# Optimization experiments

Measured on AMD Instinct MI355X. Metric: run time of the kernel, lower is better.

The kernel has to match this reference:

```python
import jax, jax.numpy as jnp
import numpy as np

N_NODES = 50000
N_EDGES = 800000
IN_DIM = 128
ADD = 8
HIDDEN = 256
OUT_DIM = 128


def gcn_conv(x, src, dst, W, b, n_nodes):
    """PyG GCNConv: linear -> sym-normalized scatter-add with self-loops -> bias."""
    loop = jnp.arange(n_nodes, dtype=src.dtype)
    s = jnp.concatenate([src, loop])
    d = jnp.concatenate([dst, loop])
    deg = jax.ops.segment_sum(jnp.ones(s.shape[0], dtype=x.dtype), d, num_segments=n_nodes)
    dinv = jnp.where(deg > 0, jax.lax.rsqrt(deg), 0.0)
    norm = dinv[s] * dinv[d]                       # [E+N]
    h = x @ W                                      # [N, F_out]
    msg = h[s] * norm[:, None]                     # [E+N, F_out]
    out = jax.ops.segment_sum(msg, d, num_segments=n_nodes)
    return out + b


def prelu(x, a):
    return jnp.where(x >= 0, x, a * x)


def setup_inputs() -> dict:
    key = jax.random.key(0)
    ks = jax.random.split(key, 8)
    x = jax.random.normal(ks[0], (N_NODES, IN_DIM), dtype=jnp.float32)
    edge_index = jax.random.randint(ks[1], (2, N_EDGES), 0, N_NODES, dtype=jnp.int64)
    id_vec = jax.random.normal(ks[2], (ADD,), dtype=jnp.float32)
    # Glorot-ish init for linear weights, PReLU slope 0.25 (torch default)
    W1 = jax.random.normal(ks[3], (IN_DIM + ADD, HIDDEN), dtype=jnp.float32) * 0.05
    b1 = jnp.zeros((HIDDEN,), dtype=jnp.float32)
    a1 = jnp.full((HIDDEN,), 0.25, dtype=jnp.float32)
    W2 = jax.random.normal(ks[4], (HIDDEN, OUT_DIM), dtype=jnp.float32) * 0.05
    b2 = jnp.zeros((OUT_DIM,), dtype=jnp.float32)
    a2 = jnp.full((OUT_DIM,), 0.25, dtype=jnp.float32)
    return {"x": x, "edge_index": edge_index, "id": id_vec,
            "W1": W1, "b1": b1, "a1": a1, "W2": W2, "b2": b2, "a2": a2}


def reference(x, edge_index, id, W1, b1, a1, W2, b2, a2):
    n = x.shape[0]
    src, dst = edge_index[0], edge_index[1]
    # tile id vector onto every node and concat along features
    xi = jnp.concatenate([x, jnp.broadcast_to(id[None, :], (n, id.shape[0]))], axis=1)
    h = gcn_conv(xi, src, dst, W1, b1, n)
    h = prelu(h, a1)
    h = gcn_conv(h, src, dst, W2, b2, n)
    h = prelu(h, a2)
    return h
```

## Files before the change

### kernel.cpp

```cpp
#include <hip/hip_runtime.h>


constexpr int NN = 50000;
constexpr int NE = 800000;
constexpr int NBUCK = 196;
constexpr int TILE = 2048;
constexpr int NSCAT = (NE + TILE - 1) / TILE;

typedef __attribute__((ext_vector_type(8))) short short8;
typedef __attribute__((ext_vector_type(4))) float floatx4;

__device__ inline void bsplit(float v, unsigned short& hi, unsigned short& lo) {
  unsigned u = __float_as_uint(v);
  hi = (unsigned short)(u >> 16);
  float rem = v - __uint_as_float(u & 0xffff0000u);
  lo = (unsigned short)(__float_as_uint(rem) >> 16);
}

__device__ inline unsigned short bf16_rtne(float v) {
  unsigned u = __float_as_uint(v);
  return (unsigned short)((u + 0x7fffu + ((u >> 16) & 1u)) >> 16);
}

__device__ inline float bflo(unsigned u) { return __uint_as_float(u << 16); }
__device__ inline float bfhi(unsigned u) { return __uint_as_float(u & 0xffff0000u); }


__global__ __launch_bounds__(256) void tile_count_kernel(const int* __restrict__ ei,
                                                         int* __restrict__ tilecnt) {
  __shared__ int h[NBUCK];
  int t = threadIdx.x;
  for (int i = t; i < NBUCK; i += 256) h[i] = 0;
  __syncthreads();
  int base = blockIdx.x * TILE;
  int end = base + TILE; if (end > NE) end = NE;
  for (int e = base + t; e < end; e += 256) atomicAdd(&h[ei[NE + e] >> 8], 1);
  __syncthreads();
  for (int i = t; i < NBUCK; i += 256) tilecnt[blockIdx.x * NBUCK + i] = h[i];
}

__global__ __launch_bounds__(256) void tile_scan_a_kernel(const int* __restrict__ tilecnt,
                                                          int* __restrict__ tpre,
                                                          int* __restrict__ bcnt) {
  __shared__ int sm[256];
  int b = blockIdx.x, t = threadIdx.x;
  int i0 = 2 * t, i1 = 2 * t + 1;
  int v0 = (i0 < NSCAT) ? tilecnt[i0 * NBUCK + b] : 0;
  int v1 = (i1 < NSCAT) ? tilecnt[i1 * NBUCK + b] : 0;
  int s = v0 + v1;
  sm[t] = s;
  __syncthreads();
  for (int off = 1; off < 256; off <<= 1) {
    int u = (t >= off) ? sm[t - off] : 0;
    __syncthreads();
    sm[t] += u;
    __syncthreads();
  }
  int ex = sm[t] - s;
  if (i0 < NSCAT) tpre[i0 * NBUCK + b] = ex;
  if (i1 < NSCAT) tpre[i1 * NBUCK + b] = ex + v0;
  if (t == 255) bcnt[b] = sm[255];
}

__global__ void bucket_base_kernel(const int* __restrict__ bcnt, int* __restrict__ bbase) {
  __shared__ int sm[256];
  int t = threadIdx.x;
  int v = (t < NBUCK) ? bcnt[t] : 0;
  sm[t] = v;
  __syncthreads();
  for (int off = 1; off < 256; off <<= 1) {
    int u = (t >= off) ? sm[t - off] : 0;
    __syncthreads();
    sm[t] += u;
    __syncthreads();
  }
  if (t < NBUCK) bbase[t] = sm[t] - v;
}

__global__ __launch_bounds__(256) void bucket_scatter_kernel(
    const int* __restrict__ ei, const int* __restrict__ tilecnt,
    const int* __restrict__ tpre, const int* __restrict__ bbase,
    unsigned* __restrict__ ebuf) {
  __shared__ int lbase[NBUCK], gb[NBUCK], lcur[NBUCK], ssc[256];
  __shared__ unsigned stage[TILE];
  int t = threadIdx.x;
  int tile = blockIdx.x;
  int base = tile * TILE;
  int cntTile = NE - base; if (cntTile > TILE) cntTile = TILE;
  int h = (t < NBUCK) ? tilecnt[tile * NBUCK + t] : 0;
  ssc[t] = h;
  __syncthreads();
  for (int off = 1; off < 256; off <<= 1) {
    int u = (t >= off) ? ssc[t - off] : 0;
    __syncthreads();
    ssc[t] += u;
    __syncthreads();
  }
  if (t < NBUCK) {
    int ex = ssc[t] - h;
    lbase[t] = ex;
    lcur[t] = ex;
    gb[t] = bbase[t] + tpre[tile * NBUCK + t];
  }
  __syncthreads();
  for (int e = base + t; e < base + cntTile; e += 256) {
    int s = ei[e];
    int d = ei[NE + e];
    int b = d >> 8;
    int pos = atomicAdd(&lcur[b], 1);
    stage[pos] = ((unsigned)(d & 255) << 16) | (unsigned)s;
  }
  __syncthreads();
  for (int i = t; i < cntTile; i += 256) {
    int lo = 0, hi = NBUCK - 1;
    while (lo < hi) {
      int mid = (lo + hi + 1) >> 1;
      if (lbase[mid] <= i) lo = mid; else hi = mid - 1;
    }
    ebuf[gb[lo] + (i - lbase[lo])] = stage[i];
  }
}

__global__ __launch_bounds__(256) void bucket_csr_kernel(
    const unsigned* __restrict__ ebuf, const int* __restrict__ bbase,
    const int* __restrict__ bcnt, int* __restrict__ offs, int* __restrict__ col,
    float* __restrict__ dinv) {
  __shared__ int cnt[256], cur[256], sums[256];
  int b = blockIdx.x, t = threadIdx.x;
  int node0 = b << 8;
  cnt[t] = 0;
  __syncthreads();
  int g0 = bbase[b], g1 = g0 + bcnt[b];
  for (int i = g0 + t; i < g1; i += 256) atomicAdd(&cnt[ebuf[i] >> 16], 1);
  __syncthreads();
  int c = cnt[t];
  sums[t] = c;
  __syncthreads();
  for (int off = 1; off < 256; off <<= 1) {
    int u = (t >= off) ? sums[t - off] : 0;
    __syncthreads();
    sums[t] += u;
    __syncthreads();
  }
  int ex = sums[t] - c;
  cur[t] = ex;
  int node = node0 + t;
  if (node < NN) {
    offs[node] = g0 + ex;
    dinv[node] = rsqrtf((float)(c + 1));
  }
  __syncthreads();
  for (int i = g0 + t; i < g1; i += 256) {
    unsigned v = ebuf[i];
    int pos = atomicAdd(&cur[v >> 16], 1);
    col[g0 + pos] = (int)(v & 0xffffu);
  }
  if (b == 0 && t == 0) offs[NN] = NE;
}

__global__ __launch_bounds__(256) void post_csr_kernel(
    const float* __restrict__ x, const float* __restrict__ dinv,
    const int* __restrict__ offs, const int* __restrict__ col,
    unsigned short* __restrict__ xsb, float* __restrict__ Svec) {
  int id = blockIdx.x * 256 + threadIdx.x;
  if (id < NN * 32) {
    float dd = dinv[id >> 5];
    float4 v = ((const float4*)x)[id];
    ushort4 o;
    o.x = bf16_rtne(v.x * dd);
    o.y = bf16_rtne(v.y * dd);
    o.z = bf16_rtne(v.z * dd);
    o.w = bf16_rtne(v.w * dd);
    ((ushort4*)xsb)[id] = o;
  } else {
    int d = id - NN * 32;
    if (d < NN) {
      float s = 0.f;
      int end = offs[d + 1];
      for (int p = offs[d]; p < end; ++p) s += dinv[col[p]];
      float dd = dinv[d];
      Svec[d] = dd * (dd + s);
    }
  }
}

template <int K, int N>
__device__ inline void pack_one(const float* __restrict__ W, unsigned short* __restrict__ Bhi,
                                unsigned short* __restrict__ Blo, int id) {
  constexpr int KC = K / 32;
  int j = id & 7;
  int lane = (id >> 3) & 63;
  int rest = id >> 9;
  int c = rest % KC;
  int nt = rest / KC;
  int k = c * 32 + (lane >> 4) * 8 + j;
  int n = nt * 16 + (lane & 15);
  unsigned short hi, lo;
  bsplit(W[(size_t)k * N + n], hi, lo);
  Bhi[id] = hi;
  Blo[id] = lo;
}

__global__ void prep_weights_kernel(const float* __restrict__ W1, const float* __restrict__ W2,
                                    const float* __restrict__ idv,
                                    unsigned short* __restrict__ B1hi, unsigned short* __restrict__ B1lo,
                                    unsigned short* __restrict__ B2hi, unsigned short* __restrict__ B2lo,
                                    float* __restrict__ cvec) {
  int id = blockIdx.x * 256 + threadIdx.x;
  if (id < 32768) {
    pack_one<128, 256>(W1, B1hi, B1lo, id);
  } else if (id < 65536) {
    pack_one<256, 128>(W2, B2hi, B2lo, id - 32768);
  } else if (id < 65536 + 256) {
    int m = id - 65536;
    float c = 0.f;
#pragma unroll
    for (int j = 0; j < 8; ++j) c += idv[j] * W1[(128 + j) * 256 + m];
    cvec[m] = c;
  }
}

template <int MODE>
__global__ __launch_bounds__(256) void agg_kernel(
    const unsigned short* __restrict__ in, const float* __restrict__ dinv,
    const int* __restrict__ offs, const int* __restrict__ col,
    const float* __restrict__ bias, const float* __restrict__ alpha,
    unsigned short* __restrict__ outhi, unsigned short* __restrict__ outlo,
    float* __restrict__ outf) {
  const uint2* inb = (const uint2*)in;
  int t = threadIdx.x;
  int node = blockIdx.x * 4 + (t >> 6);
  int lane = t & 63;
  int r = lane & 31;
  int half = lane >> 5;
  int beg = offs[node], end = offs[node + 1];

  float4 a0 = make_float4(0.f, 0.f, 0.f, 0.f);
  float4 a1 = make_float4(0.f, 0.f, 0.f, 0.f);
  float4 a2 = make_float4(0.f, 0.f, 0.f, 0.f);
  float4 a3 = make_float4(0.f, 0.f, 0.f, 0.f);
  int p = beg + half;
  for (; p + 14 < end; p += 16) {
    int s0 = col[p];      int s1 = col[p + 2];
    int s2 = col[p + 4];  int s3 = col[p + 6];
    int s4 = col[p + 8];  int s5 = col[p + 10];
    int s6 = col[p + 12]; int s7 = col[p + 14];
    uint2 v0 = inb[(size_t)s0 * 32 + r];
    uint2 v1 = inb[(size_t)s1 * 32 + r];
    uint2 v2 = inb[(size_t)s2 * 32 + r];
    uint2 v3 = inb[(size_t)s3 * 32 + r];
    uint2 v4 = inb[(size_t)s4 * 32 + r];
    uint2 v5 = inb[(size_t)s5 * 32 + r];
    uint2 v6 = inb[(size_t)s6 * 32 + r];
    uint2 v7 = inb[(size_t)s7 * 32 + r];
    a0.x += bflo(v0.x); a0.y += bfhi(v0.x); a0.z += bflo(v0.y); a0.w += bfhi(v0.y);
    a1.x += bflo(v1.x); a1.y += bfhi(v1.x); a1.z += bflo(v1.y); a1.w += bfhi(v1.y);
    a2.x += bflo(v2.x); a2.y += bfhi(v2.x); a2.z += bflo(v2.y); a2.w += bfhi(v2.y);
    a3.x += bflo(v3.x); a3.y += bfhi(v3.x); a3.z += bflo(v3.y); a3.w += bfhi(v3.y);
    a0.x += bflo(v4.x); a0.y += bfhi(v4.x); a0.z += bflo(v4.y); a0.w += bfhi(v4.y);
    a1.x += bflo(v5.x); a1.y += bfhi(v5.x); a1.z += bflo(v5.y); a1.w += bfhi(v5.y);
    a2.x += bflo(v6.x); a2.y += bfhi(v6.x); a2.z += bflo(v6.y); a2.w += bfhi(v6.y);
    a3.x += bflo(v7.x); a3.y += bfhi(v7.x); a3.z += bflo(v7.y); a3.w += bfhi(v7.y);
  }
  for (; p + 2 < end; p += 4) {
    int s0 = col[p];
    int s1 = col[p + 2];
    uint2 v0 = inb[(size_t)s0 * 32 + r];
    uint2 v1 = inb[(size_t)s1 * 32 + r];
    a0.x += bflo(v0.x); a0.y += bfhi(v0.x); a0.z += bflo(v0.y); a0.w += bfhi(v0.y);
    a1.x += bflo(v1.x); a1.y += bfhi(v1.x); a1.z += bflo(v1.y); a1.w += bfhi(v1.y);
  }
  if (p < end) {
    uint2 v0 = inb[(size_t)col[p] * 32 + r];
    a0.x += bflo(v0.x); a0.y += bfhi(v0.x); a0.z += bflo(v0.y); a0.w += bfhi(v0.y);
  }
  float4 acc = make_float4((a0.x + a1.x) + (a2.x + a3.x), (a0.y + a1.y) + (a2.y + a3.y),
                           (a0.z + a1.z) + (a2.z + a3.z), (a0.w + a1.w) + (a2.w + a3.w));
  acc.x += __shfl_xor(acc.x, 32);
  acc.y += __shfl_xor(acc.y, 32);
  acc.z += __shfl_xor(acc.z, 32);
  acc.w += __shfl_xor(acc.w, 32);

  float dd = dinv[node];
  if (half == 0) {
    uint2 sv = inb[(size_t)node * 32 + r];
    acc.x = dd * (acc.x + bflo(sv.x));
    acc.y = dd * (acc.y + bfhi(sv.x));
    acc.z = dd * (acc.z + bflo(sv.y));
    acc.w = dd * (acc.w + bfhi(sv.y));
    if (MODE == 0) {
      ushort4 h4, l4;
      bsplit(acc.x, h4.x, l4.x);
      bsplit(acc.y, h4.y, l4.y);
      bsplit(acc.z, h4.z, l4.z);
      bsplit(acc.w, h4.w, l4.w);
      ((ushort4*)outhi)[(size_t)node * 32 + r] = h4;
      ((ushort4*)outlo)[(size_t)node * 32 + r] = l4;
    } else {
      float4 b = ((const float4*)bias)[r];
      float4 al = ((const float4*)alpha)[r];
      acc.x += b.x; acc.y += b.y; acc.z += b.z; acc.w += b.w;
      acc.x = (acc.x >= 0.f) ? acc.x : al.x * acc.x;
      acc.y = (acc.y >= 0.f) ? acc.y : al.y * acc.y;
      acc.z = (acc.z >= 0.f) ? acc.z : al.z * acc.z;
      acc.w = (acc.w >= 0.f) ? acc.w : al.w * acc.w;
      ((float4*)outf)[(size_t)node * 32 + r] = acc;
    }
  }
}

__global__ __launch_bounds__(256) void gemm_fused_kernel(
    const unsigned short* __restrict__ Ahi, const unsigned short* __restrict__ Alo,
    const unsigned short* __restrict__ B1hi, const unsigned short* __restrict__ B1lo,
    const unsigned short* __restrict__ B2hi, const unsigned short* __restrict__ B2lo,
    const float* __restrict__ Svec, const float* __restrict__ cvec,
    const float* __restrict__ bias, const float* __restrict__ alpha,
    const float* __restrict__ dinv, unsigned short* __restrict__ h2b) {
  constexpr int K1 = 128, KC1 = 4, NT1 = 16;
  constexpr int KC2 = 8, NT2 = 8;
  __shared__ __attribute__((aligned(16))) char smem[4 * 16384];

  int wave = threadIdx.x >> 6;
  int lane = threadIdx.x & 63;
  int row0 = blockIdx.x * 64 + wave * 16;
  if (row0 >= NN) return;
  int m = lane & 15, quad = lane >> 4;
  char* wb = smem + wave * 16384;

  short8 ah[KC1], al[KC1];
  const unsigned short* ap = Ahi + (size_t)(row0 + m) * K1 + quad * 8;
  const unsigned short* alp = Alo + (size_t)(row0 + m) * K1 + quad * 8;
#pragma unroll
  for (int c = 0; c < KC1; ++c) {
    ah[c] = *(const short8*)(ap + c * 32);
    al[c] = *(const short8*)(alp + c * 32);
  }
  float sv[4];
#pragma unroll
  for (int i = 0; i < 4; ++i) sv[i] = Svec[row0 + quad * 4 + i];

#pragma unroll 1
  for (int nt = 0; nt < NT1; ++nt) {
    floatx4 acc = {0.f, 0.f, 0.f, 0.f};
#pragma unroll
    for (int c = 0; c < KC1; ++c) {
      short8 bh = *(const short8*)(B1hi + ((size_t)(nt * KC1 + c) * 64 + lane) * 8);
      short8 bl = *(const short8*)(B1lo + ((size_t)(nt * KC1 + c) * 64 + lane) * 8);
      acc = __builtin_amdgcn_mfma_f32_16x16x32_bf16(ah[c], bh, acc, 0, 0, 0);
      acc = __builtin_amdgcn_mfma_f32_16x16x32_bf16(ah[c], bl, acc, 0, 0, 0);
      acc = __builtin_amdgcn_mfma_f32_16x16x32_bf16(al[c], bh, acc, 0, 0, 0);
    }
    int c0 = nt * 16 + m;
    float cv = cvec[c0], bb = bias[c0], aa = alpha[c0];
#pragma unroll
    for (int i = 0; i < 4; ++i) {
      float v = acc[i] + sv[i] * cv + bb;
      v = (v >= 0.f) ? v : aa * v;
      unsigned short hi, lo;
      bsplit(v, hi, lo);
      int row16 = quad * 4 + i;
      int off = row16 * 512 + ((c0 * 2) ^ ((row16 & 7) << 4));
      *(unsigned short*)(wb + off) = hi;
      *(unsigned short*)(wb + 8192 + off) = lo;
    }
  }

  short8 ah2[KC2], al2[KC2];
#pragma unroll
  for (int c = 0; c < KC2; ++c) {
    int off = m * 512 + ((c * 64 + quad * 16) ^ ((m & 7) << 4));
    ah2[c] = *(const short8*)(wb + off);
    al2[c] = *(const short8*)(wb + 8192 + off);
  }
  float dv[4];
#pragma unroll
  for (int i = 0; i < 4; ++i) dv[i] = dinv[row0 + quad * 4 + i];

#pragma unroll 1
  for (int nt = 0; nt < NT2; ++nt) {
    floatx4 acc = {0.f, 0.f, 0.f, 0.f};
#pragma unroll
    for (int c = 0; c < KC2; ++c) {
      short8 bh = *(const short8*)(B2hi + ((size_t)(nt * KC2 + c) * 64 + lane) * 8);
      short8 bl = *(const short8*)(B2lo + ((size_t)(nt * KC2 + c) * 64 + lane) * 8);
      acc = __builtin_amdgcn_mfma_f32_16x16x32_bf16(ah2[c], bh, acc, 0, 0, 0);
      acc = __builtin_amdgcn_mfma_f32_16x16x32_bf16(ah2[c], bl, acc, 0, 0, 0);
      acc = __builtin_amdgcn_mfma_f32_16x16x32_bf16(al2[c], bh, acc, 0, 0, 0);
    }
    int c0 = nt * 16 + m;
#pragma unroll
    for (int i = 0; i < 4; ++i) {
      int r = row0 + quad * 4 + i;
      h2b[(size_t)r * 128 + c0] = bf16_rtne(acc[i] * dv[i]);
    }
  }
}

extern "C" void kernel_launch(void* const* d_in, const int* in_sizes, int n_in,
                              void* d_out, int out_size, void* d_ws, size_t ws_size,
                              hipStream_t stream) {
  const float* x = (const float*)d_in[0];
  const int* ei = (const int*)d_in[1];
  const float* idv = (const float*)d_in[2];
  const float* W1 = (const float*)d_in[3];
  const float* b1 = (const float*)d_in[4];
  const float* a1 = (const float*)d_in[5];
  const float* W2 = (const float*)d_in[6];
  const float* b2 = (const float*)d_in[7];
  const float* a2 = (const float*)d_in[8];
  float* out = (float*)d_out;

  char* w = (char*)d_ws;
  size_t off = 0;
  auto alloc = [&](size_t bytes) -> void* {
    void* p = w + off;
    off += bytes;
    off = (off + 255) & ~(size_t)255;
    return p;
  };
  int* tilecnt = (int*)alloc((size_t)NSCAT * NBUCK * 4);
  int* tpre = (int*)alloc((size_t)NSCAT * NBUCK * 4);
  int* bbase = (int*)alloc((size_t)NBUCK * 4);
  int* bcnt = (int*)alloc((size_t)NBUCK * 4);
  unsigned* ebuf = (unsigned*)alloc((size_t)NE * 4);
  float* dinv = (float*)alloc((size_t)NN * 4);
  float* Svec = (float*)alloc((size_t)NN * 4);
  int* offs = (int*)alloc((size_t)(NN + 1) * 4);
  int* col = (int*)alloc((size_t)NE * 4);
  float* cvec = (float*)alloc(256 * 4);
  unsigned short* xsb = (unsigned short*)alloc((size_t)NN * 128 * 2);
  unsigned short* aggxhi = (unsigned short*)alloc((size_t)NN * 128 * 2);
  unsigned short* aggxlo = (unsigned short*)alloc((size_t)NN * 128 * 2);
  unsigned short* h2b = (unsigned short*)alloc((size_t)NN * 128 * 2);
  unsigned short* B1hi = (unsigned short*)alloc(128 * 256 * 2);
  unsigned short* B1lo = (unsigned short*)alloc(128 * 256 * 2);
  unsigned short* B2hi = (unsigned short*)alloc(256 * 128 * 2);
  unsigned short* B2lo = (unsigned short*)alloc(256 * 128 * 2);

  tile_count_kernel<<<NSCAT, 256, 0, stream>>>(ei, tilecnt);
  tile_scan_a_kernel<<<NBUCK, 256, 0, stream>>>(tilecnt, tpre, bcnt);
  bucket_base_kernel<<<1, 256, 0, stream>>>(bcnt, bbase);
  bucket_scatter_kernel<<<NSCAT, 256, 0, stream>>>(ei, tilecnt, tpre, bbase, ebuf);
  bucket_csr_kernel<<<NBUCK, 256, 0, stream>>>(ebuf, bbase, bcnt, offs, col, dinv);

  prep_weights_kernel<<<(65536 + 256 + 255) / 256, 256, 0, stream>>>(
      W1, W2, idv, B1hi, B1lo, B2hi, B2lo, cvec);
  post_csr_kernel<<<(NN * 32 + NN + 255) / 256, 256, 0, stream>>>(
      x, dinv, offs, col, xsb, Svec);

  agg_kernel<0><<<NN / 4, 256, 0, stream>>>(xsb, dinv, offs, col, nullptr, nullptr,
                                            aggxhi, aggxlo, nullptr);

  gemm_fused_kernel<<<(NN + 63) / 64, 256, 0, stream>>>(
      aggxhi, aggxlo, B1hi, B1lo, B2hi, B2lo, Svec, cvec, b1, a1, dinv, h2b);

  agg_kernel<1><<<NN / 4, 256, 0, stream>>>(h2b, dinv, offs, col, b2, a2,
                                            nullptr, nullptr, out);
}
```

Measured before the change: 256.4 us.

## Fuse graph preprocessing kernels to cut launches and intermediate passes

Folds weight packing into the tile-count kernel and replaces the separate bucket-base scan with a redundant in-block scan of bucket counts inside the scatter and CSR kernels. The x-scaling and bf16 conversion moves into the bucket CSR kernel, which reads dinv from shared memory, and the Svec computation moves into the first aggregation kernel. This removes three kernel launches and their serialization gaps. In exchange, the x conversion now runs on only 196 blocks with a non-unrolled loop, which may lower memory-level parallelism for that pass.

```diff
diff --git a/kernel.cpp b/kernel.cpp
--- a/kernel.cpp
+++ b/kernel.cpp
@@ -24,165 +24,6 @@
 
 __device__ inline float bflo(unsigned u) { return __uint_as_float(u << 16); }
 __device__ inline float bfhi(unsigned u) { return __uint_as_float(u & 0xffff0000u); }
-
-
-__global__ __launch_bounds__(256) void tile_count_kernel(const int* __restrict__ ei,
-                                                         int* __restrict__ tilecnt) {
-  __shared__ int h[NBUCK];
-  int t = threadIdx.x;
-  for (int i = t; i < NBUCK; i += 256) h[i] = 0;
-  __syncthreads();
-  int base = blockIdx.x * TILE;
-  int end = base + TILE; if (end > NE) end = NE;
-  for (int e = base + t; e < end; e += 256) atomicAdd(&h[ei[NE + e] >> 8], 1);
-  __syncthreads();
-  for (int i = t; i < NBUCK; i += 256) tilecnt[blockIdx.x * NBUCK + i] = h[i];
-}
-
-__global__ __launch_bounds__(256) void tile_scan_a_kernel(const int* __restrict__ tilecnt,
-                                                          int* __restrict__ tpre,
-                                                          int* __restrict__ bcnt) {
-  __shared__ int sm[256];
-  int b = blockIdx.x, t = threadIdx.x;
-  int i0 = 2 * t, i1 = 2 * t + 1;
-  int v0 = (i0 < NSCAT) ? tilecnt[i0 * NBUCK + b] : 0;
-  int v1 = (i1 < NSCAT) ? tilecnt[i1 * NBUCK + b] : 0;
-  int s = v0 + v1;
-  sm[t] = s;
-  __syncthreads();
-  for (int off = 1; off < 256; off <<= 1) {
-    int u = (t >= off) ? sm[t - off] : 0;
-    __syncthreads();
-    sm[t] += u;
-    __syncthreads();
-  }
-  int ex = sm[t] - s;
-  if (i0 < NSCAT) tpre[i0 * NBUCK + b] = ex;
-  if (i1 < NSCAT) tpre[i1 * NBUCK + b] = ex + v0;
-  if (t == 255) bcnt[b] = sm[255];
-}
-
-__global__ void bucket_base_kernel(const int* __restrict__ bcnt, int* __restrict__ bbase) {
-  __shared__ int sm[256];
-  int t = threadIdx.x;
-  int v = (t < NBUCK) ? bcnt[t] : 0;
-  sm[t] = v;
-  __syncthreads();
-  for (int off = 1; off < 256; off <<= 1) {
-    int u = (t >= off) ? sm[t - off] : 0;
-    __syncthreads();
-    sm[t] += u;
-    __syncthreads();
-  }
-  if (t < NBUCK) bbase[t] = sm[t] - v;
-}
-
-__global__ __launch_bounds__(256) void bucket_scatter_kernel(
-    const int* __restrict__ ei, const int* __restrict__ tilecnt,
-    const int* __restrict__ tpre, const int* __restrict__ bbase,
-    unsigned* __restrict__ ebuf) {
-  __shared__ int lbase[NBUCK], gb[NBUCK], lcur[NBUCK], ssc[256];
-  __shared__ unsigned stage[TILE];
-  int t = threadIdx.x;
-  int tile = blockIdx.x;
-  int base = tile * TILE;
-  int cntTile = NE - base; if (cntTile > TILE) cntTile = TILE;
-  int h = (t < NBUCK) ? tilecnt[tile * NBUCK + t] : 0;
-  ssc[t] = h;
-  __syncthreads();
-  for (int off = 1; off < 256; off <<= 1) {
-    int u = (t >= off) ? ssc[t - off] : 0;
-    __syncthreads();
-    ssc[t] += u;
-    __syncthreads();
-  }
-  if (t < NBUCK) {
-    int ex = ssc[t] - h;
-    lbase[t] = ex;
-    lcur[t] = ex;
-    gb[t] = bbase[t] + tpre[tile * NBUCK + t];
-  }
-  __syncthreads();
-  for (int e = base + t; e < base + cntTile; e += 256) {
-    int s = ei[e];
-    int d = ei[NE + e];
-    int b = d >> 8;
-    int pos = atomicAdd(&lcur[b], 1);
-    stage[pos] = ((unsigned)(d & 255) << 16) | (unsigned)s;
-  }
-  __syncthreads();
-  for (int i = t; i < cntTile; i += 256) {
-    int lo = 0, hi = NBUCK - 1;
-    while (lo < hi) {
-      int mid = (lo + hi + 1) >> 1;
-      if (lbase[mid] <= i) lo = mid; else hi = mid - 1;
-    }
-    ebuf[gb[lo] + (i - lbase[lo])] = stage[i];
-  }
-}
-
-__global__ __launch_bounds__(256) void bucket_csr_kernel(
-    const unsigned* __restrict__ ebuf, const int* __restrict__ bbase,
-    const int* __restrict__ bcnt, int* __restrict__ offs, int* __restrict__ col,
-    float* __restrict__ dinv) {
-  __shared__ int cnt[256], cur[256], sums[256];
-  int b = blockIdx.x, t = threadIdx.x;
-  int node0 = b << 8;
-  cnt[t] = 0;
-  __syncthreads();
-  int g0 = bbase[b], g1 = g0 + bcnt[b];
-  for (int i = g0 + t; i < g1; i += 256) atomicAdd(&cnt[ebuf[i] >> 16], 1);
-  __syncthreads();
-  int c = cnt[t];
-  sums[t] = c;
-  __syncthreads();
-  for (int off = 1; off < 256; off <<= 1) {
-    int u = (t >= off) ? sums[t - off] : 0;
-    __syncthreads();
-    sums[t] += u;
-    __syncthreads();
-  }
-  int ex = sums[t] - c;
-  cur[t] = ex;
-  int node = node0 + t;
-  if (node < NN) {
-    offs[node] = g0 + ex;
-    dinv[node] = rsqrtf((float)(c + 1));
-  }
-  __syncthreads();
-  for (int i = g0 + t; i < g1; i += 256) {
-    unsigned v = ebuf[i];
-    int pos = atomicAdd(&cur[v >> 16], 1);
-    col[g0 + pos] = (int)(v & 0xffffu);
-  }
-  if (b == 0 && t == 0) offs[NN] = NE;
-}
-
-__global__ __launch_bounds__(256) void post_csr_kernel(
-    const float* __restrict__ x, const float* __restrict__ dinv,
-    const int* __restrict__ offs, const int* __restrict__ col,
-    unsigned short* __restrict__ xsb, float* __restrict__ Svec) {
-  int id = blockIdx.x * 256 + threadIdx.x;
-  if (id < NN * 32) {
-    float dd = dinv[id >> 5];
-    float4 v = ((const float4*)x)[id];
-    ushort4 o;
-    o.x = bf16_rtne(v.x * dd);
-    o.y = bf16_rtne(v.y * dd);
-    o.z = bf16_rtne(v.z * dd);
-    o.w = bf16_rtne(v.w * dd);
-    ((ushort4*)xsb)[id] = o;
-  } else {
-    int d = id - NN * 32;
-    if (d < NN) {
-      float s = 0.f;
-      int end = offs[d + 1];
-      for (int p = offs[d]; p < end; ++p) s += dinv[col[p]];
-      float dd = dinv[d];
-      Svec[d] = dd * (dd + s);
-    }
-  }
-}
 
 template <int K, int N>
 __device__ inline void pack_one(const float* __restrict__ W, unsigned short* __restrict__ Bhi,
@@ -201,12 +42,17 @@
   Blo[id] = lo;
 }
 
-__global__ void prep_weights_kernel(const float* __restrict__ W1, const float* __restrict__ W2,
-                                    const float* __restrict__ idv,
-                                    unsigned short* __restrict__ B1hi, unsigned short* __restrict__ B1lo,
-                                    unsigned short* __restrict__ B2hi, unsigned short* __restrict__ B2lo,
-                                    float* __restrict__ cvec) {
-  int id = blockIdx.x * 256 + threadIdx.x;
+
+__global__ __launch_bounds__(256) void tile_count_kernel(
+    const int* __restrict__ ei, int* __restrict__ tilecnt,
+    const float* __restrict__ W1, const float* __restrict__ W2,
+    const float* __restrict__ idv,
+    unsigned short* __restrict__ B1hi, unsigned short* __restrict__ B1lo,
+    unsigned short* __restrict__ B2hi, unsigned short* __restrict__ B2lo,
+    float* __restrict__ cvec) {
+  __shared__ int h[NBUCK];
+  int t = threadIdx.x;
+  int id = blockIdx.x * 256 + t;
   if (id < 32768) {
     pack_one<128, 256>(W1, B1hi, B1lo, id);
   } else if (id < 65536) {
@@ -218,6 +64,159 @@
     for (int j = 0; j < 8; ++j) c += idv[j] * W1[(128 + j) * 256 + m];
     cvec[m] = c;
   }
+  for (int i = t; i < NBUCK; i += 256) h[i] = 0;
+  __syncthreads();
+  int base = blockIdx.x * TILE;
+  int end = base + TILE; if (end > NE) end = NE;
+  for (int e = base + t; e < end; e += 256) atomicAdd(&h[ei[NE + e] >> 8], 1);
+  __syncthreads();
+  for (int i = t; i < NBUCK; i += 256) tilecnt[blockIdx.x * NBUCK + i] = h[i];
+}
+
+__global__ __launch_bounds__(256) void tile_scan_a_kernel(const int* __restrict__ tilecnt,
+                                                          int* __restrict__ tpre,
+                                                          int* __restrict__ bcnt) {
+  __shared__ int sm[256];
+  int b = blockIdx.x, t = threadIdx.x;
+  int i0 = 2 * t, i1 = 2 * t + 1;
+  int v0 = (i0 < NSCAT) ? tilecnt[i0 * NBUCK + b] : 0;
+  int v1 = (i1 < NSCAT) ? tilecnt[i1 * NBUCK + b] : 0;
+  int s = v0 + v1;
+  sm[t] = s;
+  __syncthreads();
+  for (int off = 1; off < 256; off <<= 1) {
+    int u = (t >= off) ? sm[t - off] : 0;
+    __syncthreads();
+    sm[t] += u;
+    __syncthreads();
+  }
+  int ex = sm[t] - s;
+  if (i0 < NSCAT) tpre[i0 * NBUCK + b] = ex;
+  if (i1 < NSCAT) tpre[i1 * NBUCK + b] = ex + v0;
+  if (t == 255) bcnt[b] = sm[255];
+}
+
+__global__ __launch_bounds__(256) void bucket_scatter_kernel(
+    const int* __restrict__ ei, const int* __restrict__ tilecnt,
+    const int* __restrict__ tpre, const int* __restrict__ bcnt,
+    unsigned* __restrict__ ebuf) {
+  __shared__ int lbase[NBUCK], gb[NBUCK], lcur[NBUCK], ssc[256], bb[256];
+  __shared__ unsigned stage[TILE];
+  int t = threadIdx.x;
+  int tile = blockIdx.x;
+  int base = tile * TILE;
+  int cntTile = NE - base; if (cntTile > TILE) cntTile = TILE;
+  int bv = (t < NBUCK) ? bcnt[t] : 0;
+  bb[t] = bv;
+  __syncthreads();
+  for (int off = 1; off < 256; off <<= 1) {
+    int u = (t >= off) ? bb[t - off] : 0;
+    __syncthreads();
+    bb[t] += u;
+    __syncthreads();
+  }
+  int bbase_t = bb[t] - bv;
+  int h = (t < NBUCK) ? tilecnt[tile * NBUCK + t] : 0;
+  ssc[t] = h;
+  __syncthreads();
+  for (int off = 1; off < 256; off <<= 1) {
+    int u = (t >= off) ? ssc[t - off] : 0;
+    __syncthreads();
+    ssc[t] += u;
+    __syncthreads();
+  }
+  if (t < NBUCK) {
+    int ex = ssc[t] - h;
+    lbase[t] = ex;
+    lcur[t] = ex;
+    gb[t] = bbase_t + tpre[tile * NBUCK + t];
+  }
+  __syncthreads();
+  for (int e = base + t; e < base + cntTile; e += 256) {
+    int s = ei[e];
+    int d = ei[NE + e];
+    int b = d >> 8;
+    int pos = atomicAdd(&lcur[b], 1);
+    stage[pos] = ((unsigned)(d & 255) << 16) | (unsigned)s;
+  }
+  __syncthreads();
+  for (int i = t; i < cntTile; i += 256) {
+    int lo = 0, hi = NBUCK - 1;
+    while (lo < hi) {
+      int mid = (lo + hi + 1) >> 1;
+      if (lbase[mid] <= i) lo = mid; else hi = mid - 1;
+    }
+    ebuf[gb[lo] + (i - lbase[lo])] = stage[i];
+  }
+}
+
+__global__ __launch_bounds__(256) void bucket_csr_kernel(
+    const unsigned* __restrict__ ebuf, const int* __restrict__ bcnt,
+    int* __restrict__ offs, int* __restrict__ col, float* __restrict__ dinv,
+    const float* __restrict__ x, unsigned short* __restrict__ xsb) {
+  __shared__ int cnt[256], cur[256], sums[256];
+  __shared__ float dvs[256];
+  int b = blockIdx.x, t = threadIdx.x;
+  int node0 = b << 8;
+  int bv = (t < NBUCK) ? bcnt[t] : 0;
+  sums[t] = bv;
+  __syncthreads();
+  for (int off = 1; off < 256; off <<= 1) {
+    int u = (t >= off) ? sums[t - off] : 0;
+    __syncthreads();
+    sums[t] += u;
+    __syncthreads();
+  }
+  int g0 = sums[b] - bcnt[b];
+  int g1 = g0 + bcnt[b];
+  __syncthreads();
+  cnt[t] = 0;
+  __syncthreads();
+  for (int i = g0 + t; i < g1; i += 256) atomicAdd(&cnt[ebuf[i] >> 16], 1);
+  __syncthreads();
+  int c = cnt[t];
+  sums[t] = c;
+  __syncthreads();
+  for (int off = 1; off < 256; off <<= 1) {
+    int u = (t >= off) ? sums[t - off] : 0;
+    __syncthreads();
+    sums[t] += u;
+    __syncthreads();
+  }
+  int ex = sums[t] - c;
+  cur[t] = ex;
+  int node = node0 + t;
+  if (node < NN) {
+    float dd = rsqrtf((float)(c + 1));
+    offs[node] = g0 + ex;
+    dinv[node] = dd;
+    dvs[t] = dd;
+  }
+  __syncthreads();
+  for (int i = g0 + t; i < g1; i += 256) {
+    unsigned v = ebuf[i];
+    int pos = atomicAdd(&cur[v >> 16], 1);
+    col[g0 + pos] = (int)(v & 0xffffu);
+  }
+  if (b == 0 && t == 0) offs[NN] = NE;
+  const float4* x4 = (const float4*)x;
+  ushort4* xb4 = (ushort4*)xsb;
+#pragma unroll 1
+  for (int i = 0; i < 32; ++i) {
+    int idx = i * 256 + t;
+    int nl = idx >> 5, el = idx & 31;
+    int n2 = node0 + nl;
+    if (n2 < NN) {
+      float dd = dvs[nl];
+      float4 v = x4[(size_t)n2 * 32 + el];
+      ushort4 o;
+      o.x = bf16_rtne(v.x * dd);
+      o.y = bf16_rtne(v.y * dd);
+      o.z = bf16_rtne(v.z * dd);
+      o.w = bf16_rtne(v.w * dd);
+      xb4[(size_t)n2 * 32 + el] = o;
+    }
+  }
 }
 
 template <int MODE>
@@ -226,9 +225,19 @@
     const int* __restrict__ offs, const int* __restrict__ col,
     const float* __restrict__ bias, const float* __restrict__ alpha,
     unsigned short* __restrict__ outhi, unsigned short* __restrict__ outlo,
-    float* __restrict__ outf) {
+    float* __restrict__ outf, float* __restrict__ Svec) {
+  int t = threadIdx.x;
+  if (MODE == 0) {
+    int d = blockIdx.x * 256 + t;
+    if (d < NN) {
+      float s = 0.f;
+      int end2 = offs[d + 1];
+      for (int p2 = offs[d]; p2 < end2; ++p2) s += dinv[col[p2]];
+      float dd2 = dinv[d];
+      Svec[d] = dd2 * (dd2 + s);
+    }
+  }
   const uint2* inb = (const uint2*)in;
-  int t = threadIdx.x;
   int node = blockIdx.x * 4 + (t >> 6);
   int lane = t & 63;
   int r = lane & 31;
@@ -420,7 +429,6 @@
   };
   int* tilecnt = (int*)alloc((size_t)NSCAT * NBUCK * 4);
   int* tpre = (int*)alloc((size_t)NSCAT * NBUCK * 4);
-  int* bbase = (int*)alloc((size_t)NBUCK * 4);
   int* bcnt = (int*)alloc((size_t)NBUCK * 4);
   unsigned* ebuf = (unsigned*)alloc((size_t)NE * 4);
   float* dinv = (float*)alloc((size_t)NN * 4);
@@ -437,23 +445,18 @@
   unsigned short* B2hi = (unsigned short*)alloc(256 * 128 * 2);
   unsigned short* B2lo = (unsigned short*)alloc(256 * 128 * 2);
 
-  tile_count_kernel<<<NSCAT, 256, 0, stream>>>(ei, tilecnt);
+  tile_count_kernel<<<NSCAT, 256, 0, stream>>>(ei, tilecnt, W1, W2, idv,
+                                               B1hi, B1lo, B2hi, B2lo, cvec);
   tile_scan_a_kernel<<<NBUCK, 256, 0, stream>>>(tilecnt, tpre, bcnt);
-  bucket_base_kernel<<<1, 256, 0, stream>>>(bcnt, bbase);
-  bucket_scatter_kernel<<<NSCAT, 256, 0, stream>>>(ei, tilecnt, tpre, bbase, ebuf);
-  bucket_csr_kernel<<<NBUCK, 256, 0, stream>>>(ebuf, bbase, bcnt, offs, col, dinv);
-
-  prep_weights_kernel<<<(65536 + 256 + 255) / 256, 256, 0, stream>>>(
-      W1, W2, idv, B1hi, B1lo, B2hi, B2lo, cvec);
-  post_csr_kernel<<<(NN * 32 + NN + 255) / 256, 256, 0, stream>>>(
-      x, dinv, offs, col, xsb, Svec);
+  bucket_scatter_kernel<<<NSCAT, 256, 0, stream>>>(ei, tilecnt, tpre, bcnt, ebuf);
+  bucket_csr_kernel<<<NBUCK, 256, 0, stream>>>(ebuf, bcnt, offs, col, dinv, x, xsb);
 
   agg_kernel<0><<<NN / 4, 256, 0, stream>>>(xsb, dinv, offs, col, nullptr, nullptr,
-                                            aggxhi, aggxlo, nullptr);
+                                            aggxhi, aggxlo, nullptr, Svec);
 
   gemm_fused_kernel<<<(NN + 63) / 64, 256, 0, stream>>>(
       aggxhi, aggxlo, B1hi, B1lo, B2hi, B2lo, Svec, cvec, b1, a1, dinv, h2b);
 
   agg_kernel<1><<<NN / 4, 256, 0, stream>>>(h2b, dinv, offs, col, b2, a2,
-                                            nullptr, nullptr, out);
-}
+                                            nullptr, nullptr, out, nullptr);
+}
```

After: 253.6 us. Within noise of the previous version (-1.1%).
